# Kernel optimization log

Measured on AMD Instinct MI355X. Metric: run time of the kernel, lower is better.

The kernel has to match this reference:

```python
import jax, jax.numpy as jnp
import numpy as np

NS, NM, NR, H = 5000, 100000, 2000, 128
E_SM, E_RM, E_SIM, L = 2_000_000, 1_000_000, 2_000_000, 500_000
NUM_LAYERS = 4  # flattened: layer-0 sage convs 0..3, layer-1 sage convs 0..3 -> stacked [2,4,...]


def _seg_sum(x, idx, n):
    return jax.ops.segment_sum(x, idx, num_segments=n)


def sage_conv(x_src, x_dst, Wl, bl, Wr, src, dst, n_dst):
    # PyG SAGEConv: mean-aggregate neighbor features, lin_l (with bias), + lin_r(root, no bias)
    agg = _seg_sum(x_src[src], dst, n_dst)                      # [n_dst, H]
    cnt = _seg_sum(jnp.ones_like(src, dtype=x_src.dtype), dst, n_dst)
    mean = agg / jnp.maximum(cnt, 1.0)[:, None]
    return mean @ Wl + bl + x_dst @ Wr


def gcn_conv(x, W, b, src, dst, n):
    # PyG GCNConv: add self loops, symmetric normalization deg^-1/2 (deg over dst incl. self loops)
    loop = jnp.arange(n, dtype=src.dtype)
    src2 = jnp.concatenate([src, loop])
    dst2 = jnp.concatenate([dst, loop])
    deg = _seg_sum(jnp.ones_like(dst2, dtype=x.dtype), dst2, n)
    dinv = jnp.where(deg > 0, jax.lax.rsqrt(deg), 0.0)
    norm = dinv[src2] * dinv[dst2]                               # [E+n]
    xw = x @ W                                                   # [n, H]
    out = _seg_sum(xw[src2] * norm[:, None], dst2, n)
    return out + b


def setup_inputs() -> dict:
    key = jax.random.key(0)
    ks = jax.random.split(key, 20)
    s = 0.05
    inp = {
        "emb_srna": jax.random.normal(ks[0], (NS, H), jnp.float32) * s,
        "emb_mrna": jax.random.normal(ks[1], (NM, H), jnp.float32) * s,
        "emb_rbp": jax.random.normal(ks[2], (NR, H), jnp.float32) * s,
        # stacked SAGE params: [layer=2, rel=4, ...]; rel order:
        # 0: srna->mrna, 1: mrna->srna (rev), 2: rbp->mrna, 3: mrna->rbp (rev)
        "sage_Wl": jax.random.normal(ks[3], (2, 4, H, H), jnp.float32) * s,
        "sage_bl": jnp.zeros((2, 4, H), jnp.float32),
        "sage_Wr": jax.random.normal(ks[4], (2, 4, H, H), jnp.float32) * s,
        # stacked GCN params: [layer=2, rel=2 (sim, rev_sim), ...]
        "gcn_W": jax.random.normal(ks[5], (2, 2, H, H), jnp.float32) * s,
        "gcn_b": jnp.zeros((2, 2, H), jnp.float32),
        "src_sm": jax.random.randint(ks[6], (E_SM,), 0, NS),
        "dst_sm": jax.random.randint(ks[7], (E_SM,), 0, NM),
        "src_rm": jax.random.randint(ks[8], (E_RM,), 0, NR),
        "dst_rm": jax.random.randint(ks[9], (E_RM,), 0, NM),
        "src_sim": jax.random.randint(ks[10], (E_SIM,), 0, NM),
        "dst_sim": jax.random.randint(ks[11], (E_SIM,), 0, NM),
        "lbl_srna": jax.random.randint(ks[12], (L,), 0, NS),
        "lbl_mrna": jax.random.randint(ks[13], (L,), 0, NM),
        "lbl_rbp": jax.random.randint(ks[14], (L,), 0, NR),
    }
    return inp


def reference(emb_srna, emb_mrna, emb_rbp, sage_Wl, sage_bl, sage_Wr, gcn_W, gcn_b,
              src_sm, dst_sm, src_rm, dst_rm, src_sim, dst_sim,
              lbl_srna, lbl_mrna, lbl_rbp):
    x_s, x_m, x_r = emb_srna, emb_mrna, emb_rbp
    for l in range(2):
        m_new = (
            sage_conv(x_s, x_m, sage_Wl[l, 0], sage_bl[l, 0], sage_Wr[l, 0], src_sm, dst_sm, NM)
            + sage_conv(x_r, x_m, sage_Wl[l, 2], sage_bl[l, 2], sage_Wr[l, 2], src_rm, dst_rm, NM)
            + gcn_conv(x_m, gcn_W[l, 0], gcn_b[l, 0], src_sim, dst_sim, NM)
            + gcn_conv(x_m, gcn_W[l, 1], gcn_b[l, 1], dst_sim, src_sim, NM)
        )
        s_new = sage_conv(x_m, x_s, sage_Wl[l, 1], sage_bl[l, 1], sage_Wr[l, 1], dst_sm, src_sm, NS)
        r_new = sage_conv(x_m, x_r, sage_Wl[l, 3], sage_bl[l, 3], sage_Wr[l, 3], dst_rm, src_rm, NR)
        x_s, x_m, x_r = jax.nn.relu(s_new), jax.nn.relu(m_new), jax.nn.relu(r_new)
    feat_m = x_m[lbl_mrna]
    pred_srna_mrna = jnp.sum(x_s[lbl_srna] * feat_m, axis=-1)
    pred_rbp_mrna = jnp.sum(x_r[lbl_rbp] * feat_m, axis=-1)
    return (pred_srna_mrna, pred_rbp_mrna)
```

## Files before the change

### kernel.cpp

```cpp
#include <hip/hip_runtime.h>
#include <hip/hip_bf16.h>

#define NSN 5000
#define NMN 100000
#define NRN 2000
#define HDIM 128
#define ESM 2000000
#define ERM 1000000
#define ESIM 2000000
#define LBL 500000

#define CNT_TOTAL (4 * NMN + NSN + NRN)
#define POOL_TOTAL (2 * ESM + 2 * ERM + 2 * ESIM)
#define NBTOT 1222
#define WCAP 14336
#define MAXNODES 512
#define MBLK 25000
#define SR_TOTAL (NSN + NRN)

typedef short bf16x8 __attribute__((ext_vector_type(8)));
typedef float f32x4 __attribute__((ext_vector_type(4)));
typedef float f32x2 __attribute__((ext_vector_type(2)));

__device__ __forceinline__ unsigned short f2bf(float f) {
  unsigned u = __float_as_uint(f);
  unsigned r = (u + 0x7fffu + ((u >> 16) & 1u)) >> 16;
  return (unsigned short)r;
}
__device__ __forceinline__ float bf_lo(unsigned v) { return __uint_as_float(v << 16); }
__device__ __forceinline__ float bf_hi(unsigned v) { return __uint_as_float(v & 0xffff0000u); }
__device__ __forceinline__ unsigned pack2(float x, float y) {
  return (unsigned)f2bf(x) | ((unsigned)f2bf(y) << 16);
}
__device__ __forceinline__ f32x2 up2(unsigned v) {
  f32x2 r;
  r.x = bf_lo(v);
  r.y = bf_hi(v);
  return r;
}
__device__ __forceinline__ void unpack8(uint4 v, float* f) {
  f[0] = bf_lo(v.x); f[1] = bf_hi(v.x);
  f[2] = bf_lo(v.y); f[3] = bf_hi(v.y);
  f[4] = bf_lo(v.z); f[5] = bf_hi(v.z);
  f[6] = bf_lo(v.w); f[7] = bf_hi(v.w);
}


__global__ void zero_int(int* __restrict__ p, int n) {
  int i = blockIdx.x * blockDim.x + threadIdx.x;
  if (i < n) p[i] = 0;
}

struct BInfo { int g; int ns; int ne; };
__device__ __forceinline__ BInfo binfo(int id) {
  BInfo bi;
  if (id < 196)       { int k = id;        bi.g = 0;                   bi.ns = k << 9; bi.ne = min(bi.ns + 512, NMN); }
  else if (id < 509)  { int k = id - 196;  bi.g = NMN;                 bi.ns = k << 4; bi.ne = min(bi.ns + 16,  NSN); }
  else if (id < 705)  { int k = id - 509;  bi.g = NMN + NSN;           bi.ns = k << 9; bi.ne = min(bi.ns + 512, NMN); }
  else if (id < 830)  { int k = id - 705;  bi.g = 2 * NMN + NSN;       bi.ns = k << 4; bi.ne = min(bi.ns + 16,  NRN); }
  else if (id < 1026) { int k = id - 830;  bi.g = 2 * NMN + NSN + NRN; bi.ns = k << 9; bi.ne = min(bi.ns + 512, NMN); }
  else                { int k = id - 1026; bi.g = 3 * NMN + NSN + NRN; bi.ns = k << 9; bi.ne = min(bi.ns + 512, NMN); }
  return bi;
}

template <int SHF, int NBF, int SHR, int NBR>
__global__ __launch_bounds__(256) void countbuckets(
    const int* __restrict__ a, const int* __restrict__ b, int n,
    int* __restrict__ bcnt, int bb) {
  __shared__ int hist[NBF + NBR];
  int tid = threadIdx.x;
  int base = blockIdx.x * 4096;
  for (int k = tid; k < NBF + NBR; k += 256) hist[k] = 0;
  __syncthreads();
  int end = min(base + 4096, n);
  for (int idx = base + tid; idx < end; idx += 256) {
    atomicAdd(&hist[b[idx] >> SHF], 1);
    atomicAdd(&hist[NBF + (a[idx] >> SHR)], 1);
  }
  __syncthreads();
  for (int k = tid; k < NBF + NBR; k += 256) {
    int c = hist[k];
    if (c) atomicAdd(&bcnt[bb + k], c);
  }
}

__global__ void scan_buckets(const int* __restrict__ bcnt, int* __restrict__ bstart,
                             int* __restrict__ bcur, int* __restrict__ off_sentinel) {
  __shared__ int buf[256];
  int t = threadIdx.x;
  int base = 0;
  for (int c0 = 0; c0 < NBTOT; c0 += 256) {
    int v = (c0 + t < NBTOT) ? bcnt[c0 + t] : 0;
    buf[t] = v; __syncthreads();
    for (int o = 1; o < 256; o <<= 1) {
      int a = (t >= o) ? buf[t - o] : 0;
      __syncthreads();
      buf[t] += a;
      __syncthreads();
    }
    if (c0 + t < NBTOT) {
      int excl = buf[t] - v + base;
      bstart[c0 + t] = excl;
      bcur[c0 + t] = excl;
    }
    base += buf[255];
    __syncthreads();
  }
  if (t == 0) { bstart[NBTOT] = base; *off_sentinel = base; }
}

template <int SHF, int NBF, int SHR, int NBR>
__global__ __launch_bounds__(256) void multisplit(
    const int* __restrict__ a, const int* __restrict__ b, int n,
    int* __restrict__ bcur, int bb, int2* __restrict__ stage) {
  __shared__ int hist[NBF + NBR];
  __shared__ int gpos[NBF + NBR];
  int tid = threadIdx.x;
  int base = blockIdx.x * 4096;
  for (int k = tid; k < NBF + NBR; k += 256) hist[k] = 0;
  __syncthreads();
  int dv[16], sv[16];
#pragma unroll
  for (int j = 0; j < 16; j++) {
    int idx = base + j * 256 + tid;
    if (idx < n) {
      sv[j] = a[idx]; dv[j] = b[idx];
      atomicAdd(&hist[dv[j] >> SHF], 1);
      atomicAdd(&hist[NBF + (sv[j] >> SHR)], 1);
    } else {
      dv[j] = -1;
    }
  }
  __syncthreads();
  for (int k = tid; k < NBF + NBR; k += 256) {
    int c = hist[k];
    gpos[k] = c ? atomicAdd(&bcur[bb + k], c) : 0;
  }
  __syncthreads();
#pragma unroll
  for (int j = 0; j < 16; j++) {
    if (dv[j] >= 0) {
      int s1 = atomicAdd(&gpos[dv[j] >> SHF], 1);
      stage[s1] = make_int2(dv[j], sv[j]);
      int s2 = atomicAdd(&gpos[NBF + (sv[j] >> SHR)], 1);
      stage[s2] = make_int2(sv[j], dv[j]);
    }
  }
}

__global__ __launch_bounds__(256) void scatter_bucket(
    const int2* __restrict__ stage, const int* __restrict__ bstart,
    int* __restrict__ cur, int* __restrict__ off, int* __restrict__ pool) {
  __shared__ int win[WCAP];
  __shared__ int hist[MAXNODES];
  __shared__ int part[256];
  int b = blockIdx.x;
  BInfo bi = binfo(b);
  int s0 = bstart[b], s1 = bstart[b + 1];
  int sz = s1 - s0, nn = bi.ne - bi.ns;
  int t = threadIdx.x;
  for (int k = t; k < nn; k += 256) hist[k] = 0;
  __syncthreads();
  for (int k = s0 + t; k < s1; k += 256)
    atomicAdd(&hist[stage[k].x - bi.ns], 1);
  __syncthreads();
  int a0 = (2 * t < nn) ? hist[2 * t] : 0;
  int a1 = (2 * t + 1 < nn) ? hist[2 * t + 1] : 0;
  part[t] = a0 + a1;
  __syncthreads();
  for (int o = 1; o < 256; o <<= 1) {
    int a = (t >= o) ? part[t - o] : 0;
    __syncthreads();
    part[t] += a;
    __syncthreads();
  }
  int e0 = part[t] - a0 - a1;
  int e1 = e0 + a0;
  if (2 * t < nn)     { off[bi.g + bi.ns + 2 * t] = s0 + e0; hist[2 * t] = e0; }
  if (2 * t + 1 < nn) { off[bi.g + bi.ns + 2 * t + 1] = s0 + e1; hist[2 * t + 1] = e1; }
  __syncthreads();
  if (sz <= WCAP) {
    for (int k = s0 + t; k < s1; k += 256) {
      int2 pr = stage[k];
      int slot = atomicAdd(&hist[pr.x - bi.ns], 1);
      win[slot] = pr.y;
    }
    __syncthreads();
    for (int k = t; k < sz; k += 256) pool[s0 + k] = win[k];
  } else {
    for (int k = s0 + t; k < s1; k += 256) {
      int2 pr = stage[k];
      int slot = atomicAdd(&cur[bi.g + pr.x], 1);
      pool[s0 + hist[pr.x - bi.ns] + slot] = pr.y;
    }
  }
}

__global__ void compute_dinv(const int* __restrict__ off1, const int* __restrict__ off2,
                             float* __restrict__ dinv1, float* __restrict__ dinv2, int n) {
  int v = blockIdx.x * blockDim.x + threadIdx.x;
  if (v < n) {
    dinv1[v] = rsqrtf((float)(off1[v + 1] - off1[v] + 1));
    dinv2[v] = rsqrtf((float)(off2[v + 1] - off2[v] + 1));
  }
}

__global__ void trans_weights(const float* __restrict__ sWl, const float* __restrict__ sWr,
                              const float* __restrict__ gW, unsigned short* __restrict__ wt) {
  int i = blockIdx.x * blockDim.x + threadIdx.x;
  if (i >= 18 * 16384) return;
  int mat = i >> 14, l = mat / 9, slot = mat % 9;
  int idx = i & 16383, nn = idx >> 7, kk = idx & 127;
  int s_ = kk * 128 + nn;
  float v;
  if (slot < 4)      v = sWl[((l * 4 + slot) << 14) + s_];
  else if (slot < 6) v = gW[((l * 2 + (slot - 4)) << 14) + s_];
  else if (slot == 6) v = sWr[((l * 4 + 0) << 14) + s_] + sWr[((l * 4 + 2) << 14) + s_];
  else if (slot == 7) v = sWr[((l * 4 + 1) << 14) + s_];
  else                v = sWr[((l * 4 + 3) << 14) + s_];
  wt[i] = f2bf(v);
}

__global__ void prep_bias(const float* __restrict__ sbl, const float* __restrict__ gb,
                          float* __restrict__ biasM) {
  int i = threadIdx.x;
  int l = i >> 7, j = i & 127;
  biasM[i] = sbl[(l * 4 + 0) * 128 + j] + sbl[(l * 4 + 2) * 128 + j] +
             gb[(l * 2 + 0) * 128 + j] + gb[(l * 2 + 1) * 128 + j];
}

__global__ void cast_all(const float2* __restrict__ es, const float2* __restrict__ em,
                         const float2* __restrict__ er, unsigned* __restrict__ os,
                         unsigned* __restrict__ om, unsigned* __restrict__ orr) {
  int i = blockIdx.x * blockDim.x + threadIdx.x;
  if (i < NSN * 64) { float2 v = es[i]; os[i] = pack2(v.x, v.y); }
  if (i < NMN * 64) { float2 v = em[i]; om[i] = pack2(v.x, v.y); }
  if (i < NRN * 64) { float2 v = er[i]; orr[i] = pack2(v.x, v.y); }
}


__device__ __forceinline__ void body_plain16(const unsigned* __restrict__ xh,
                                             const int* __restrict__ pool,
                                             int i0, int q, f32x2* acc) {
  int u1 = pool[i0 + q], u2 = pool[i0 + 4 + q];
  int u3 = pool[i0 + 8 + q], u4 = pool[i0 + 12 + q];
  uint4 a = *(const uint4*)(xh + (size_t)u1 * 64);
  uint4 b = *(const uint4*)(xh + (size_t)u2 * 64);
  uint4 c = *(const uint4*)(xh + (size_t)u3 * 64);
  uint4 d = *(const uint4*)(xh + (size_t)u4 * 64);
  acc[0] += up2(a.x) * 1.f + up2(b.x) * 1.f + up2(c.x) * 1.f + up2(d.x) * 1.f;
  acc[1] += up2(a.y) * 1.f + up2(b.y) * 1.f + up2(c.y) * 1.f + up2(d.y) * 1.f;
  acc[2] += up2(a.z) * 1.f + up2(b.z) * 1.f + up2(c.z) * 1.f + up2(d.z) * 1.f;
  acc[3] += up2(a.w) * 1.f + up2(b.w) * 1.f + up2(c.w) * 1.f + up2(d.w) * 1.f;
}

__device__ __forceinline__ void body_gcn16(const unsigned* __restrict__ xh,
                                           const int* __restrict__ pool,
                                           const float* __restrict__ dinv,
                                           int i0, int q, f32x2* acc) {
  int u1 = pool[i0 + q], u2 = pool[i0 + 4 + q];
  int u3 = pool[i0 + 8 + q], u4 = pool[i0 + 12 + q];
  uint4 a = *(const uint4*)(xh + (size_t)u1 * 64);
  uint4 b = *(const uint4*)(xh + (size_t)u2 * 64);
  uint4 c = *(const uint4*)(xh + (size_t)u3 * 64);
  uint4 d = *(const uint4*)(xh + (size_t)u4 * 64);
  float s1 = dinv[u1], s2 = dinv[u2], s3 = dinv[u3], s4 = dinv[u4];
  acc[0] += up2(a.x) * s1 + up2(b.x) * s2 + up2(c.x) * s3 + up2(d.x) * s4;
  acc[1] += up2(a.y) * s1 + up2(b.y) * s2 + up2(c.y) * s3 + up2(d.y) * s4;
  acc[2] += up2(a.z) * s1 + up2(b.z) * s2 + up2(c.z) * s3 + up2(d.z) * s4;
  acc[3] += up2(a.w) * s1 + up2(b.w) * s2 + up2(c.w) * s3 + up2(d.w) * s4;
}

__device__ __forceinline__ void tail_plain16(const unsigned* __restrict__ xh,
                                             const int* __restrict__ pool,
                                             int i0, int e, int q, f32x2* acc) {
  int i1 = i0 + q, i2 = i0 + 4 + q, i3 = i0 + 8 + q, i4 = i0 + 12 + q;
  int u1 = pool[min(i1, e - 1)], u2 = pool[min(i2, e - 1)];
  int u3 = pool[min(i3, e - 1)], u4 = pool[min(i4, e - 1)];
  uint4 a = *(const uint4*)(xh + (size_t)u1 * 64);
  uint4 b = *(const uint4*)(xh + (size_t)u2 * 64);
  uint4 c = *(const uint4*)(xh + (size_t)u3 * 64);
  uint4 d = *(const uint4*)(xh + (size_t)u4 * 64);
  float s1 = (i1 < e) ? 1.f : 0.f, s2 = (i2 < e) ? 1.f : 0.f;
  float s3 = (i3 < e) ? 1.f : 0.f, s4 = (i4 < e) ? 1.f : 0.f;
  acc[0] += up2(a.x) * s1 + up2(b.x) * s2 + up2(c.x) * s3 + up2(d.x) * s4;
  acc[1] += up2(a.y) * s1 + up2(b.y) * s2 + up2(c.y) * s3 + up2(d.y) * s4;
  acc[2] += up2(a.z) * s1 + up2(b.z) * s2 + up2(c.z) * s3 + up2(d.z) * s4;
  acc[3] += up2(a.w) * s1 + up2(b.w) * s2 + up2(c.w) * s3 + up2(d.w) * s4;
}

__device__ __forceinline__ void tail_gcn16(const unsigned* __restrict__ xh,
                                           const int* __restrict__ pool,
                                           const float* __restrict__ dinv,
                                           int i0, int e, int q, f32x2* acc) {
  int i1 = i0 + q, i2 = i0 + 4 + q, i3 = i0 + 8 + q, i4 = i0 + 12 + q;
  int u1 = pool[min(i1, e - 1)], u2 = pool[min(i2, e - 1)];
  int u3 = pool[min(i3, e - 1)], u4 = pool[min(i4, e - 1)];
  uint4 a = *(const uint4*)(xh + (size_t)u1 * 64);
  uint4 b = *(const uint4*)(xh + (size_t)u2 * 64);
  uint4 c = *(const uint4*)(xh + (size_t)u3 * 64);
  uint4 d = *(const uint4*)(xh + (size_t)u4 * 64);
  float s1 = (i1 < e) ? dinv[u1] : 0.f, s2 = (i2 < e) ? dinv[u2] : 0.f;
  float s3 = (i3 < e) ? dinv[u3] : 0.f, s4 = (i4 < e) ? dinv[u4] : 0.f;
  acc[0] += up2(a.x) * s1 + up2(b.x) * s2 + up2(c.x) * s3 + up2(d.x) * s4;
  acc[1] += up2(a.y) * s1 + up2(b.y) * s2 + up2(c.y) * s3 + up2(d.y) * s4;
  acc[2] += up2(a.z) * s1 + up2(b.z) * s2 + up2(c.z) * s3 + up2(d.z) * s4;
  acc[3] += up2(a.w) * s1 + up2(b.w) * s2 + up2(c.w) * s3 + up2(d.w) * s4;
}

__device__ __forceinline__ void wave_reduce2(f32x2* acc) {
#pragma unroll
  for (int j = 0; j < 4; j++) {
    acc[j].x += __shfl_xor(acc[j].x, 16, 64);
    acc[j].y += __shfl_xor(acc[j].y, 16, 64);
    acc[j].x += __shfl_xor(acc[j].x, 32, 64);
    acc[j].y += __shfl_xor(acc[j].y, 32, 64);
  }
}

__device__ __forceinline__ uint4 pack_scaled(const f32x2* acc, float sc) {
  uint4 o;
  o.x = pack2(acc[0].x * sc, acc[0].y * sc);
  o.y = pack2(acc[1].x * sc, acc[1].y * sc);
  o.z = pack2(acc[2].x * sc, acc[2].y * sc);
  o.w = pack2(acc[3].x * sc, acc[3].y * sc);
  return o;
}

__global__ __launch_bounds__(256) void agg_all(
    const unsigned* __restrict__ xs, const unsigned* __restrict__ xm,
    const unsigned* __restrict__ xr, const int* __restrict__ pool,
    const int* __restrict__ off_sm, const int* __restrict__ off_rm,
    const int* __restrict__ off_si, const int* __restrict__ off_si2,
    const int* __restrict__ off_ms, const int* __restrict__ off_mr,
    const float* __restrict__ dinv1, const float* __restrict__ dinv2,
    unsigned* __restrict__ aggA, unsigned* __restrict__ aggB,
    unsigned* __restrict__ aggC, unsigned* __restrict__ aggD,
    unsigned* __restrict__ aggS, unsigned* __restrict__ aggR) {
  __shared__ float psum[3][128];
  int b = blockIdx.x;
  int lane = threadIdx.x & 63;
  int q = lane >> 4, h = lane & 15;

  int k4 = b >> 2, r4 = b & 3;
  bool is_sr = (r4 == 3) && (k4 < SR_TOTAL);

  if (!is_sr) {
    int mb = b - min(k4 + ((r4 == 3) ? 1 : 0), SR_TOTAL);
    int w = mb * 4 + (threadIdx.x >> 6);
    if (w >= NMN) return;
    const unsigned* xsh = xs + h * 4;
    const unsigned* xmh = xm + h * 4;
    const unsigned* xrh = xr + h * 4;
    f32x2 acc[4];
    {
      int s = off_sm[w], e = off_sm[w + 1];
      int nb = (e - s) & ~15;
#pragma unroll
      for (int j = 0; j < 4; j++) acc[j] = (f32x2)(0.f);
      int i0 = s;
      for (; i0 < s + nb; i0 += 16) body_plain16(xsh, pool, i0, q, acc);
      if (i0 < e) tail_plain16(xsh, pool, i0, e, q, acc);
      wave_reduce2(acc);
      if (q == 0) {
        float inv = (e > s) ? 1.0f / (float)(e - s) : 0.0f;
        *(uint4*)(aggA + (size_t)w * 64 + h * 4) = pack_scaled(acc, inv);
      }
    }
    {
      int s = off_rm[w], e = off_rm[w + 1];
      int nb = (e - s) & ~15;
#pragma unroll
      for (int j = 0; j < 4; j++) acc[j] = (f32x2)(0.f);
      int i0 = s;
      for (; i0 < s + nb; i0 += 16) body_plain16(xrh, pool, i0, q, acc);
      if (i0 < e) tail_plain16(xrh, pool, i0, e, q, acc);
      wave_reduce2(acc);
      if (q == 0) {
        float inv = (e > s) ? 1.0f / (float)(e - s) : 0.0f;
        *(uint4*)(aggB + (size_t)w * 64 + h * 4) = pack_scaled(acc, inv);
      }
    }
    {
      int s = off_si[w], e = off_si[w + 1];
      int nb = (e - s) & ~15;
#pragma unroll
      for (int j = 0; j < 4; j++) acc[j] = (f32x2)(0.f);
      int i0 = s;
      for (; i0 < s + nb; i0 += 16) body_gcn16(xmh, pool, dinv1, i0, q, acc);
      if (i0 < e) tail_gcn16(xmh, pool, dinv1, i0, e, q, acc);
      wave_reduce2(acc);
      if (q == 0) {
        float dw = dinv1[w];
        uint4 xv = *(const uint4*)(xmh + (size_t)w * 64);
        f32x2 fx[4] = {up2(xv.x), up2(xv.y), up2(xv.z), up2(xv.w)};
        float dw2 = dw * dw;
        uint4 o;
        f32x2 r0 = acc[0] * dw + fx[0] * dw2, r1 = acc[1] * dw + fx[1] * dw2;
        f32x2 r2 = acc[2] * dw + fx[2] * dw2, r3 = acc[3] * dw + fx[3] * dw2;
        o.x = pack2(r0.x, r0.y); o.y = pack2(r1.x, r1.y);
        o.z = pack2(r2.x, r2.y); o.w = pack2(r3.x, r3.y);
        *(uint4*)(aggC + (size_t)w * 64 + h * 4) = o;
      }
    }
    {
      int s = off_si2[w], e = off_si2[w + 1];
      int nb = (e - s) & ~15;
#pragma unroll
      for (int j = 0; j < 4; j++) acc[j] = (f32x2)(0.f);
      int i0 = s;
      for (; i0 < s + nb; i0 += 16) body_gcn16(xmh, pool, dinv2, i0, q, acc);
      if (i0 < e) tail_gcn16(xmh, pool, dinv2, i0, e, q, acc);
      wave_reduce2(acc);
      if (q == 0) {
        float dw = dinv2[w];
        uint4 xv = *(const uint4*)(xmh + (size_t)w * 64);
        f32x2 fx[4] = {up2(xv.x), up2(xv.y), up2(xv.z), up2(xv.w)};
        float dw2 = dw * dw;
        uint4 o;
        f32x2 r0 = acc[0] * dw + fx[0] * dw2, r1 = acc[1] * dw + fx[1] * dw2;
        f32x2 r2 = acc[2] * dw + fx[2] * dw2, r3 = acc[3] * dw + fx[3] * dw2;
        o.x = pack2(r0.x, r0.y); o.y = pack2(r1.x, r1.y);
        o.z = pack2(r2.x, r2.y); o.w = pack2(r3.x, r3.y);
        *(uint4*)(aggD + (size_t)w * 64 + h * 4) = o;
      }
    }
  } else {
    int sr = k4;
    int node;
    const int* offp;
    unsigned* outb;
    if (sr < NSN) { node = sr; offp = off_ms; outb = aggS; }
    else          { node = sr - NSN; offp = off_mr; outb = aggR; }
    const unsigned* xmh = xm + h * 4;
    int sub = threadIdx.x >> 6;
    int s = offp[node], e = offp[node + 1];
    f32x2 acc[4];
#pragma unroll
    for (int j = 0; j < 4; j++) acc[j] = (f32x2)(0.f);
    int i0 = s + sub * 16;
    for (; i0 + 16 <= e; i0 += 64) body_plain16(xmh, pool, i0, q, acc);
    if (i0 < e) tail_plain16(xmh, pool, i0, e, q, acc);
    wave_reduce2(acc);
    if (sub && q == 0) {
#pragma unroll
      for (int j = 0; j < 4; j++) {
        psum[sub - 1][h * 8 + 2 * j] = acc[j].x;
        psum[sub - 1][h * 8 + 2 * j + 1] = acc[j].y;
      }
    }
    __syncthreads();
    if (sub == 0 && q == 0) {
#pragma unroll
      for (int j = 0; j < 4; j++) {
        acc[j].x += psum[0][h * 8 + 2 * j] + psum[1][h * 8 + 2 * j] + psum[2][h * 8 + 2 * j];
        acc[j].y += psum[0][h * 8 + 2 * j + 1] + psum[1][h * 8 + 2 * j + 1] + psum[2][h * 8 + 2 * j + 1];
      }
      float inv = (e > s) ? 1.0f / (float)(e - s) : 0.0f;
      *(uint4*)(outb + (size_t)node * 64 + h * 4) = pack_scaled(acc, inv);
    }
  }
}


#define LDA 136

__global__ __launch_bounds__(256) void gemm_mfma(
    const unsigned short* __restrict__ a0, const unsigned short* __restrict__ w0,
    const unsigned short* __restrict__ a1, const unsigned short* __restrict__ w1,
    const unsigned short* __restrict__ a2, const unsigned short* __restrict__ w2,
    const unsigned short* __restrict__ a3, const unsigned short* __restrict__ w3,
    const unsigned short* __restrict__ a4, const unsigned short* __restrict__ w4,
    const float* __restrict__ bias, unsigned short* __restrict__ out, int n) {
  __shared__ __align__(16) unsigned short As[64 * LDA];
  __shared__ __align__(16) unsigned short Ws[128 * LDA];

  int tid = threadIdx.x;
  int w = tid >> 6, lane = tid & 63;
  int q = lane >> 4, c = lane & 15;
  int r0 = blockIdx.x * 64;

  const unsigned short* Ap[5] = {a0, a1, a2, a3, a4};
  const unsigned short* Wp[5] = {w0, w1, w2, w3, w4};

  float bias_v[8];
#pragma unroll
  for (int n0 = 0; n0 < 8; n0++) bias_v[n0] = bias[n0 * 16 + c];

  f32x4 acc[8];
#pragma unroll
  for (int n0 = 0; n0 < 8; n0++) acc[n0] = (f32x4){0.f, 0.f, 0.f, 0.f};

  for (int p = 0; p < 5; p++) {
    if (!Ap[p]) continue;
    __syncthreads();
    for (int j = tid; j < 2048; j += 256) {
      int row = j >> 4, colc = (j & 15) * 8;
      *(uint4*)&Ws[row * LDA + colc] = *(const uint4*)(Wp[p] + row * 128 + colc);
    }
    for (int j = tid; j < 1024; j += 256) {
      int row = j >> 4, colc = (j & 15) * 8;
      uint4 v = make_uint4(0u, 0u, 0u, 0u);
      if (r0 + row < n) v = *(const uint4*)(Ap[p] + (size_t)(r0 + row) * 128 + colc);
      *(uint4*)&As[row * LDA + colc] = v;
    }
    __syncthreads();

    int arow = (w * 16 + c) * LDA;
#pragma unroll
    for (int k0 = 0; k0 < 128; k0 += 32) {
      bf16x8 af = *(const bf16x8*)&As[arow + k0 + q * 8];
#pragma unroll
      for (int n0 = 0; n0 < 8; n0++) {
        bf16x8 bfv = *(const bf16x8*)&Ws[(n0 * 16 + c) * LDA + k0 + q * 8];
        acc[n0] = __builtin_amdgcn_mfma_f32_16x16x32_bf16(af, bfv, acc[n0], 0, 0, 0);
      }
    }
  }

  __syncthreads();
#pragma unroll
  for (int n0 = 0; n0 < 8; n0++) {
#pragma unroll
    for (int reg = 0; reg < 4; reg++) {
      float v = acc[n0][reg] + bias_v[n0];
      v = fmaxf(v, 0.f);
      As[(w * 16 + q * 4 + reg) * LDA + n0 * 16 + c] = f2bf(v);
    }
  }
  __syncthreads();
  for (int j = tid; j < 1024; j += 256) {
    int row = j >> 4, colc = (j & 15) * 8;
    if (r0 + row < n)
      *(uint4*)(out + (size_t)(r0 + row) * 128 + colc) = *(const uint4*)&As[row * LDA + colc];
  }
}


__global__ void dots_kernel(const unsigned* __restrict__ xs, const unsigned* __restrict__ xm,
                            const unsigned* __restrict__ xr, const int* __restrict__ ls,
                            const int* __restrict__ lm, const int* __restrict__ lr,
                            float* __restrict__ out) {
  int wv = (blockIdx.x * blockDim.x + threadIdx.x) >> 6;
  int lane = threadIdx.x & 63;
  int q = lane >> 4, h = lane & 15;
  int i = wv * 4 + q;
  if (i >= LBL) return;
  int im = lm[i], is = ls[i], ir = lr[i];
  uint4 mv = *(const uint4*)(xm + (size_t)im * 64 + h * 4);
  uint4 sv = *(const uint4*)(xs + (size_t)is * 64 + h * 4);
  uint4 rv = *(const uint4*)(xr + (size_t)ir * 64 + h * 4);
  float fm[8], fs[8], fr[8];
  unpack8(mv, fm); unpack8(sv, fs); unpack8(rv, fr);
  float p1 = 0.f, p2 = 0.f;
#pragma unroll
  for (int j = 0; j < 8; j++) { p1 = fmaf(fs[j], fm[j], p1); p2 = fmaf(fr[j], fm[j], p2); }
#pragma unroll
  for (int m = 1; m < 16; m <<= 1) {
    p1 += __shfl_xor(p1, m, 64);
    p2 += __shfl_xor(p2, m, 64);
  }
  if (h == 0) { out[i] = p1; out[LBL + i] = p2; }
}


extern "C" void kernel_launch(void* const* d_in, const int* in_sizes, int n_in,
                              void* d_out, int out_size, void* d_ws, size_t ws_size,
                              hipStream_t stream) {
  const float* emb_s = (const float*)d_in[0];
  const float* emb_m = (const float*)d_in[1];
  const float* emb_r = (const float*)d_in[2];
  const float* sWl = (const float*)d_in[3];
  const float* sbl = (const float*)d_in[4];
  const float* sWr = (const float*)d_in[5];
  const float* gW  = (const float*)d_in[6];
  const float* gb  = (const float*)d_in[7];
  const int* src_sm  = (const int*)d_in[8];
  const int* dst_sm  = (const int*)d_in[9];
  const int* src_rm  = (const int*)d_in[10];
  const int* dst_rm  = (const int*)d_in[11];
  const int* src_sim = (const int*)d_in[12];
  const int* dst_sim = (const int*)d_in[13];
  const int* lbl_s = (const int*)d_in[14];
  const int* lbl_m = (const int*)d_in[15];
  const int* lbl_r = (const int*)d_in[16];
  float* out = (float*)d_out;

  char* p = (char*)d_ws;
  auto alloc = [&](size_t bytes) -> char* {
    char* r = p;
    p += (bytes + 255) & ~(size_t)255;
    return r;
  };

  int* cnt_base = (int*)alloc(sizeof(int) * CNT_TOTAL);

  int* off_base = (int*)alloc(sizeof(int) * (CNT_TOTAL + 1));
  int* off_sm  = off_base;
  int* off_ms  = off_sm + NMN;
  int* off_rm  = off_ms + NSN;
  int* off_mr  = off_rm + NMN;
  int* off_si  = off_mr + NRN;
  int* off_si2 = off_si + NMN;

  int* bcnt   = (int*)alloc(sizeof(int) * 1280);
  int* bstart = (int*)alloc(sizeof(int) * 1280);
  int* bcur   = (int*)alloc(sizeof(int) * 1280);
  int* pool = (int*)alloc(sizeof(int) * POOL_TOTAL);

  float* dinv1 = (float*)alloc(sizeof(float) * NMN);
  float* dinv2 = (float*)alloc(sizeof(float) * NMN);

  unsigned* xsb = (unsigned*)alloc(sizeof(unsigned) * (size_t)NSN * 64);
  unsigned* xmb = (unsigned*)alloc(sizeof(unsigned) * (size_t)NMN * 64);
  unsigned* xrb = (unsigned*)alloc(sizeof(unsigned) * (size_t)NRN * 64);
  unsigned* xs0 = (unsigned*)alloc(sizeof(unsigned) * (size_t)NSN * 64);
  unsigned* xs1 = (unsigned*)alloc(sizeof(unsigned) * (size_t)NSN * 64);
  unsigned* xm0 = (unsigned*)alloc(sizeof(unsigned) * (size_t)NMN * 64);
  unsigned* xm1 = (unsigned*)alloc(sizeof(unsigned) * (size_t)NMN * 64);
  unsigned* xr0 = (unsigned*)alloc(sizeof(unsigned) * (size_t)NRN * 64);
  unsigned* xr1 = (unsigned*)alloc(sizeof(unsigned) * (size_t)NRN * 64);
  unsigned* aggA = (unsigned*)alloc(sizeof(unsigned) * (size_t)NMN * 64);
  unsigned* aggB = (unsigned*)alloc(sizeof(unsigned) * (size_t)NMN * 64);
  unsigned* aggC = (unsigned*)alloc(sizeof(unsigned) * (size_t)NMN * 64);
  unsigned* aggD = (unsigned*)alloc(sizeof(unsigned) * (size_t)NMN * 64);
  unsigned* aggS = (unsigned*)alloc(sizeof(unsigned) * (size_t)NSN * 64);
  unsigned* aggR = (unsigned*)alloc(sizeof(unsigned) * (size_t)NRN * 64);

  unsigned short* wt = (unsigned short*)alloc(sizeof(unsigned short) * 18 * 16384);
  float* biasM = (float*)alloc(sizeof(float) * 2 * 128);

  int2* stage = (int2*)aggA;

  auto WT = [&](int l, int slot) -> const unsigned short* {
    return wt + (((size_t)l * 9 + slot) << 14);
  };

  zero_int<<<5, 256, 0, stream>>>(bcnt, 1280);
  countbuckets<9, 196, 4, 313><<<(ESM + 4095) / 4096, 256, 0, stream>>>(
      src_sm, dst_sm, ESM, bcnt, 0);
  countbuckets<9, 196, 4, 125><<<(ERM + 4095) / 4096, 256, 0, stream>>>(
      src_rm, dst_rm, ERM, bcnt, 509);
  countbuckets<9, 196, 9, 196><<<(ESIM + 4095) / 4096, 256, 0, stream>>>(
      src_sim, dst_sim, ESIM, bcnt, 830);
  scan_buckets<<<1, 256, 0, stream>>>(bcnt, bstart, bcur, off_base + CNT_TOTAL);

  multisplit<9, 196, 4, 313><<<(ESM + 4095) / 4096, 256, 0, stream>>>(
      src_sm, dst_sm, ESM, bcur, 0, stage);
  multisplit<9, 196, 4, 125><<<(ERM + 4095) / 4096, 256, 0, stream>>>(
      src_rm, dst_rm, ERM, bcur, 509, stage);
  multisplit<9, 196, 9, 196><<<(ESIM + 4095) / 4096, 256, 0, stream>>>(
      src_sim, dst_sim, ESIM, bcur, 830, stage);
  zero_int<<<(CNT_TOTAL + 255) / 256, 256, 0, stream>>>(cnt_base, CNT_TOTAL);
  scatter_bucket<<<NBTOT, 256, 0, stream>>>(stage, bstart, cnt_base, off_base, pool);

  compute_dinv<<<(NMN + 255) / 256, 256, 0, stream>>>(off_si, off_si2, dinv1, dinv2, NMN);
  trans_weights<<<(18 * 16384 + 255) / 256, 256, 0, stream>>>(sWl, sWr, gW, wt);
  prep_bias<<<1, 256, 0, stream>>>(sbl, gb, biasM);
  cast_all<<<(NMN * 64 + 255) / 256, 256, 0, stream>>>((const float2*)emb_s, (const float2*)emb_m,
                                                       (const float2*)emb_r, xsb, xmb, xrb);

  const int AGG_GRID = MBLK + SR_TOTAL;
  for (int l = 0; l < 2; ++l) {
    const unsigned* xs_c = l ? xs0 : xsb;
    const unsigned* xm_c = l ? xm0 : xmb;
    const unsigned* xr_c = l ? xr0 : xrb;
    unsigned* xs_n = l ? xs1 : xs0;
    unsigned* xm_n = l ? xm1 : xm0;
    unsigned* xr_n = l ? xr1 : xr0;

    agg_all<<<AGG_GRID, 256, 0, stream>>>(
        xs_c, xm_c, xr_c, pool, off_sm, off_rm, off_si, off_si2, off_ms, off_mr,
        dinv1, dinv2, aggA, aggB, aggC, aggD, aggS, aggR);

    gemm_mfma<<<(NMN + 63) / 64, 256, 0, stream>>>(
        (const unsigned short*)aggA, WT(l, 0), (const unsigned short*)aggB, WT(l, 2),
        (const unsigned short*)aggC, WT(l, 4), (const unsigned short*)aggD, WT(l, 5),
        (const unsigned short*)xm_c, WT(l, 6), biasM + l * 128,
        (unsigned short*)xm_n, NMN);
    gemm_mfma<<<(NSN + 63) / 64, 256, 0, stream>>>(
        (const unsigned short*)aggS, WT(l, 1), (const unsigned short*)xs_c, WT(l, 7),
        nullptr, nullptr, nullptr, nullptr, nullptr, nullptr,
        sbl + (l * 4 + 1) * 128, (unsigned short*)xs_n, NSN);
    gemm_mfma<<<(NRN + 63) / 64, 256, 0, stream>>>(
        (const unsigned short*)aggR, WT(l, 3), (const unsigned short*)xr_c, WT(l, 8),
        nullptr, nullptr, nullptr, nullptr, nullptr, nullptr,
        sbl + (l * 4 + 3) * 128, (unsigned short*)xr_n, NRN);
  }

  dots_kernel<<<(LBL * 16 + 255) / 256, 256, 0, stream>>>(xs1, xm1, xr1, lbl_s, lbl_m, lbl_r, out);
}
```

Measured before the change: 1.157 ms.

## Drop bucket counting pass by using fixed-capacity staging buckets

Removes the separate count-buckets and scan pass that ran before the multisplit. Each bucket now gets a fixed-capacity region in the staging buffer, and the cursors start at those fixed offsets. A scan of the final cursor positions then produces the compacted bucket starts, and scatter_bucket reads its entries from the padded regions. This saves one full read of all edge index arrays plus the histogram atomics, but nothing checks for overflow: a bucket that exceeds its hardcoded capacity would silently corrupt its neighbour, so correctness depends on the input degree distribution.

```diff
diff --git a/kernel.cpp b/kernel.cpp
--- a/kernel.cpp
+++ b/kernel.cpp
@@ -17,6 +17,19 @@
 #define MAXNODES 512
 #define MBLK 25000
 #define SR_TOTAL (NSN + NRN)
+
+#define CAP0 12288
+#define CAP1 8192
+#define CAP2 7168
+#define CAP3 9216
+#define CAP4 12288
+#define CAP5 12288
+#define PB0 0
+#define PB1 (PB0 + 196 * CAP0)
+#define PB2 (PB1 + 313 * CAP1)
+#define PB3 (PB2 + 196 * CAP2)
+#define PB4 (PB3 + 125 * CAP3)
+#define PB5 (PB4 + 196 * CAP4)
 
 typedef short bf16x8 __attribute__((ext_vector_type(8)));
 typedef float f32x4 __attribute__((ext_vector_type(4)));
@@ -63,50 +76,18 @@
   return bi;
 }
 
-template <int SHF, int NBF, int SHR, int NBR>
-__global__ __launch_bounds__(256) void countbuckets(
-    const int* __restrict__ a, const int* __restrict__ b, int n,
-    int* __restrict__ bcnt, int bb) {
-  __shared__ int hist[NBF + NBR];
-  int tid = threadIdx.x;
-  int base = blockIdx.x * 4096;
-  for (int k = tid; k < NBF + NBR; k += 256) hist[k] = 0;
-  __syncthreads();
-  int end = min(base + 4096, n);
-  for (int idx = base + tid; idx < end; idx += 256) {
-    atomicAdd(&hist[b[idx] >> SHF], 1);
-    atomicAdd(&hist[NBF + (a[idx] >> SHR)], 1);
-  }
-  __syncthreads();
-  for (int k = tid; k < NBF + NBR; k += 256) {
-    int c = hist[k];
-    if (c) atomicAdd(&bcnt[bb + k], c);
-  }
-}
-
-__global__ void scan_buckets(const int* __restrict__ bcnt, int* __restrict__ bstart,
-                             int* __restrict__ bcur, int* __restrict__ off_sentinel) {
-  __shared__ int buf[256];
-  int t = threadIdx.x;
-  int base = 0;
-  for (int c0 = 0; c0 < NBTOT; c0 += 256) {
-    int v = (c0 + t < NBTOT) ? bcnt[c0 + t] : 0;
-    buf[t] = v; __syncthreads();
-    for (int o = 1; o < 256; o <<= 1) {
-      int a = (t >= o) ? buf[t - o] : 0;
-      __syncthreads();
-      buf[t] += a;
-      __syncthreads();
-    }
-    if (c0 + t < NBTOT) {
-      int excl = buf[t] - v + base;
-      bstart[c0 + t] = excl;
-      bcur[c0 + t] = excl;
-    }
-    base += buf[255];
-    __syncthreads();
-  }
-  if (t == 0) { bstart[NBTOT] = base; *off_sentinel = base; }
+__device__ __forceinline__ int pstart(int id) {
+  if (id < 196)       return PB0 + id * CAP0;
+  else if (id < 509)  return PB1 + (id - 196) * CAP1;
+  else if (id < 705)  return PB2 + (id - 509) * CAP2;
+  else if (id < 830)  return PB3 + (id - 705) * CAP3;
+  else if (id < 1026) return PB4 + (id - 830) * CAP4;
+  else                return PB5 + (id - 1026) * CAP5;
+}
+
+__global__ void init_pcur(int* __restrict__ bcur) {
+  int id = blockIdx.x * blockDim.x + threadIdx.x;
+  if (id < NBTOT) bcur[id] = pstart(id);
 }
 
 template <int SHF, int NBF, int SHR, int NBR>
@@ -148,6 +129,28 @@
   }
 }
 
+__global__ void scan_counts(const int* __restrict__ bcur, int* __restrict__ bstart,
+                            int* __restrict__ off_sentinel) {
+  __shared__ int buf[256];
+  int t = threadIdx.x;
+  int base = 0;
+  for (int c0 = 0; c0 < NBTOT; c0 += 256) {
+    int id = c0 + t;
+    int v = (id < NBTOT) ? (bcur[id] - pstart(id)) : 0;
+    buf[t] = v; __syncthreads();
+    for (int o = 1; o < 256; o <<= 1) {
+      int a = (t >= o) ? buf[t - o] : 0;
+      __syncthreads();
+      buf[t] += a;
+      __syncthreads();
+    }
+    if (id < NBTOT) bstart[id] = buf[t] - v + base;
+    base += buf[255];
+    __syncthreads();
+  }
+  if (t == 0) { bstart[NBTOT] = base; *off_sentinel = base; }
+}
+
 __global__ __launch_bounds__(256) void scatter_bucket(
     const int2* __restrict__ stage, const int* __restrict__ bstart,
     int* __restrict__ cur, int* __restrict__ off, int* __restrict__ pool) {
@@ -156,13 +159,15 @@
   __shared__ int part[256];
   int b = blockIdx.x;
   BInfo bi = binfo(b);
-  int s0 = bstart[b], s1 = bstart[b + 1];
-  int sz = s1 - s0, nn = bi.ne - bi.ns;
+  int p0 = pstart(b);
+  int d0 = bstart[b];
+  int sz = bstart[b + 1] - d0;
+  int nn = bi.ne - bi.ns;
   int t = threadIdx.x;
   for (int k = t; k < nn; k += 256) hist[k] = 0;
   __syncthreads();
-  for (int k = s0 + t; k < s1; k += 256)
-    atomicAdd(&hist[stage[k].x - bi.ns], 1);
+  for (int k = t; k < sz; k += 256)
+    atomicAdd(&hist[stage[p0 + k].x - bi.ns], 1);
   __syncthreads();
   int a0 = (2 * t < nn) ? hist[2 * t] : 0;
   int a1 = (2 * t + 1 < nn) ? hist[2 * t + 1] : 0;
@@ -176,22 +181,22 @@
   }
   int e0 = part[t] - a0 - a1;
   int e1 = e0 + a0;
-  if (2 * t < nn)     { off[bi.g + bi.ns + 2 * t] = s0 + e0; hist[2 * t] = e0; }
-  if (2 * t + 1 < nn) { off[bi.g + bi.ns + 2 * t + 1] = s0 + e1; hist[2 * t + 1] = e1; }
+  if (2 * t < nn)     { off[bi.g + bi.ns + 2 * t] = d0 + e0; hist[2 * t] = e0; }
+  if (2 * t + 1 < nn) { off[bi.g + bi.ns + 2 * t + 1] = d0 + e1; hist[2 * t + 1] = e1; }
   __syncthreads();
   if (sz <= WCAP) {
-    for (int k = s0 + t; k < s1; k += 256) {
-      int2 pr = stage[k];
+    for (int k = t; k < sz; k += 256) {
+      int2 pr = stage[p0 + k];
       int slot = atomicAdd(&hist[pr.x - bi.ns], 1);
       win[slot] = pr.y;
     }
     __syncthreads();
-    for (int k = t; k < sz; k += 256) pool[s0 + k] = win[k];
+    for (int k = t; k < sz; k += 256) pool[d0 + k] = win[k];
   } else {
-    for (int k = s0 + t; k < s1; k += 256) {
-      int2 pr = stage[k];
+    for (int k = t; k < sz; k += 256) {
+      int2 pr = stage[p0 + k];
       int slot = atomicAdd(&cur[bi.g + pr.x], 1);
-      pool[s0 + hist[pr.x - bi.ns] + slot] = pr.y;
+      pool[d0 + hist[pr.x - bi.ns] + slot] = pr.y;
     }
   }
 }
@@ -603,7 +608,6 @@
   int* off_si  = off_mr + NRN;
   int* off_si2 = off_si + NMN;
 
-  int* bcnt   = (int*)alloc(sizeof(int) * 1280);
   int* bstart = (int*)alloc(sizeof(int) * 1280);
   int* bcur   = (int*)alloc(sizeof(int) * 1280);
   int* pool = (int*)alloc(sizeof(int) * POOL_TOTAL);
@@ -636,21 +640,14 @@
     return wt + (((size_t)l * 9 + slot) << 14);
   };
 
-  zero_int<<<5, 256, 0, stream>>>(bcnt, 1280);
-  countbuckets<9, 196, 4, 313><<<(ESM + 4095) / 4096, 256, 0, stream>>>(
-      src_sm, dst_sm, ESM, bcnt, 0);
-  countbuckets<9, 196, 4, 125><<<(ERM + 4095) / 4096, 256, 0, stream>>>(
-      src_rm, dst_rm, ERM, bcnt, 509);
-  countbuckets<9, 196, 9, 196><<<(ESIM + 4095) / 4096, 256, 0, stream>>>(
-      src_sim, dst_sim, ESIM, bcnt, 830);
-  scan_buckets<<<1, 256, 0, stream>>>(bcnt, bstart, bcur, off_base + CNT_TOTAL);
-
+  init_pcur<<<(NBTOT + 255) / 256, 256, 0, stream>>>(bcur);
   multisplit<9, 196, 4, 313><<<(ESM + 4095) / 4096, 256, 0, stream>>>(
       src_sm, dst_sm, ESM, bcur, 0, stage);
   multisplit<9, 196, 4, 125><<<(ERM + 4095) / 4096, 256, 0, stream>>>(
       src_rm, dst_rm, ERM, bcur, 509, stage);
   multisplit<9, 196, 9, 196><<<(ESIM + 4095) / 4096, 256, 0, stream>>>(
       src_sim, dst_sim, ESIM, bcur, 830, stage);
+  scan_counts<<<1, 256, 0, stream>>>(bcur, bstart, off_base + CNT_TOTAL);
   zero_int<<<(CNT_TOTAL + 255) / 256, 256, 0, stream>>>(cnt_base, CNT_TOTAL);
   scatter_bucket<<<NBTOT, 256, 0, stream>>>(stage, bstart, cnt_base, off_base, pool);
 
```

New measurement: 1.096 ms. 1.06x faster.
